# Optimization experiments

Hardware: AMD Instinct MI355X
Metric: run time of the kernel (lower is better)

The kernel has to match this reference:

```python
import jax, jax.numpy as jnp
import numpy as np

B, N, A, O, D, Q, H = 64, 4, 1024, 128, 256, 256, 128
NEG_INF = -1e30


def setup_inputs() -> dict:
    key = jax.random.key(0)
    ks = jax.random.split(key, 8)
    q = jax.random.normal(ks[0], (B, N, 1, Q), dtype=jnp.float32)
    att1 = jax.random.uniform(ks[1], (B, N, A, O), dtype=jnp.float32)
    obj_reps = jax.random.normal(ks[2], (B, O, D), dtype=jnp.float32)
    tags_attention = jax.random.randint(ks[3], (B, N, A), 0, 2, dtype=jnp.int32)
    W1 = jax.random.normal(ks[4], (D + Q, H), dtype=jnp.float32) / np.sqrt(D + Q)
    b1 = jnp.zeros((H,), dtype=jnp.float32)
    W2 = jax.random.normal(ks[5], (H, 1), dtype=jnp.float32) / np.sqrt(H)
    b2 = jnp.zeros((1,), dtype=jnp.float32)
    return {"q": q, "att1": att1, "obj_reps": obj_reps,
            "tags_attention": tags_attention,
            "W1": W1, "b1": b1, "W2": W2, "b2": b2, "t": 1}


def reference(q, att1, obj_reps, tags_attention, W1, b1, W2, b2, t):
    # v: [B,N,A,D] = att1 [B,N,A,O] @ obj_reps [B,O,D]
    v = jnp.einsum('bnao,bod->bnad', att1, obj_reps)
    # q broadcast over token dim A, concat -> [B,N,A,D+Q]
    q_proj = jnp.broadcast_to(q, v.shape[:3] + (q.shape[-1],))
    vq = jnp.concatenate([v, q_proj], axis=-1)
    # FCNet: Linear + ReLU (dropout is identity at inference)
    joint_repr = jax.nn.relu(vq @ W1 + b1)          # [B,N,A,H]
    logits = (joint_repr @ W2 + b2)[..., 0]          # [B,N,A]
    # temperature-scaled masked softmax over tokens
    masked = jnp.where(tags_attention > 0, logits / t, NEG_INF)
    att2 = jax.nn.softmax(masked, axis=-1)           # [B,N,A]
    # attention_last: [B,N,O] = att2 [B,N,1,A] @ att1 [B,N,A,O]
    return jnp.einsum('bna,bnao->bno', att2, att1)
```

## Files before the change

### kernel.cpp

```cpp
#include <hip/hip_runtime.h>
#include <math.h>

#define Bc 64
#define Nc 4
#define Ac 1024
#define Oc 128
#define Dc 256
#define Qc 256
#define Hc 128
#define BN (Bc*Nc)

using f4     = __attribute__((ext_vector_type(4))) float;
using f32x4  = __attribute__((ext_vector_type(4))) float;
using short8 = __attribute__((ext_vector_type(8))) short;
using us4    = __attribute__((ext_vector_type(4))) unsigned short;

__device__ inline float decode_t(const void* p) {
    int i = *(const int*)p;
    if (i >= 1 && i <= 1000000) return (float)i;
    return __int_as_float(i);
}

__device__ inline void split_bf16(float x, unsigned short& hi, unsigned short& lo) {
    unsigned u = __builtin_bit_cast(unsigned, x);
    hi = (unsigned short)(u >> 16);
    float hif = __builtin_bit_cast(float, u & 0xFFFF0000u);
    float lof = x - hif;
    lo = (unsigned short)(__builtin_bit_cast(unsigned, lof) >> 16);
}

__global__ __launch_bounds__(256) void prep_M_kernel(
    const float* __restrict__ obj, const float* __restrict__ W1,
    unsigned short* __restrict__ Mt_hi, unsigned short* __restrict__ Mt_lo)
{
    __shared__ float w_s[32][36];
    __shared__ float obj_sT[32][68];

    const int t  = threadIdx.x;
    const int tx = t & 15;
    const int ty = t >> 4;
    const int h0 = blockIdx.x * 32;
    const int o0 = blockIdx.y * 64;
    const int b  = blockIdx.z;

    float acc[2][4];
    #pragma unroll
    for (int i = 0; i < 2; i++)
        #pragma unroll
        for (int j = 0; j < 4; j++) acc[i][j] = 0.f;

    for (int ko = 0; ko < 8; ++ko) {
        __syncthreads();
        {
            int r = t >> 3, c4 = t & 7;
            f4 v = *(const f4*)(W1 + (size_t)(ko * 32 + r) * Hc + h0 + c4 * 4);
            *(f4*)&w_s[r][c4 * 4] = v;
        }
        #pragma unroll
        for (int s = 0; s < 2; s++) {
            int idx = t + 256 * s;
            int r = idx >> 3, c4 = idx & 7;
            f4 v = *(const f4*)(obj + ((size_t)b * Oc + o0 + r) * Dc + ko * 32 + c4 * 4);
            obj_sT[c4 * 4 + 0][r] = v[0];
            obj_sT[c4 * 4 + 1][r] = v[1];
            obj_sT[c4 * 4 + 2][r] = v[2];
            obj_sT[c4 * 4 + 3][r] = v[3];
        }
        __syncthreads();
        #pragma unroll 4
        for (int k = 0; k < 32; k++) {
            float a0 = w_s[k][ty * 2];
            float a1 = w_s[k][ty * 2 + 1];
            f4 bv = *(const f4*)&obj_sT[k][tx * 4];
            #pragma unroll
            for (int j = 0; j < 4; j++) {
                acc[0][j] += a0 * bv[j];
                acc[1][j] += a1 * bv[j];
            }
        }
    }

    #pragma unroll
    for (int i = 0; i < 2; i++) {
        us4 hi, lo;
        #pragma unroll
        for (int j = 0; j < 4; j++) {
            unsigned short h16, l16;
            split_bf16(acc[i][j], h16, l16);
            hi[j] = h16; lo[j] = l16;
        }
        size_t ofs = ((size_t)b * Hc + h0 + ty * 2 + i) * Oc + o0 + tx * 4;
        *(us4*)(Mt_hi + ofs) = hi;
        *(us4*)(Mt_lo + ofs) = lo;
    }
}

__global__ __launch_bounds__(512) void prep_qb_kernel(
    const float* __restrict__ q, const float* __restrict__ W1,
    const float* __restrict__ b1, float* __restrict__ qb,
    float* __restrict__ out_acc, float* __restrict__ Zsum)
{
    __shared__ float qs[256];
    __shared__ float red[4][128];
    const int t = threadIdx.x;
    const int bn = blockIdx.x;

    if (t < 256) qs[t] = q[bn * Qc + t];
    __syncthreads();

    const int h = t & 127, kq = t >> 7;
    float acc = 0.f;
    const float* w = W1 + (size_t)(Dc + kq * 64) * Hc + h;
    #pragma unroll 8
    for (int d = 0; d < 64; ++d)
        acc += qs[kq * 64 + d] * w[(size_t)d * Hc];
    red[kq][h] = acc;
    __syncthreads();

    if (t < 128) {
        qb[bn * Hc + t] = b1[t] + red[0][t] + red[1][t] + red[2][t] + red[3][t];
        out_acc[bn * Oc + t] = 0.f;
    }
    if (t == 128) Zsum[bn] = 0.f;
}

__global__ __launch_bounds__(256) void main_kernel(
    const float* __restrict__ att1, const int* __restrict__ tags,
    const unsigned short* __restrict__ Mt_hi, const unsigned short* __restrict__ Mt_lo,
    const float* __restrict__ qb, const float* __restrict__ W2,
    const float* __restrict__ b2, const void* __restrict__ tptr,
    float* __restrict__ out_acc, float* __restrict__ Zsum)
{
    __shared__ unsigned short A_hi[64][136];
    __shared__ unsigned short A_lo[64][136];
    __shared__ float part2[64][4];
    __shared__ float qb_s[128], w2_s[128];
    __shared__ float e_s[64];

    const int t    = threadIdx.x;
    const int wave = t >> 6;
    const int lane = t & 63;
    const int l15  = lane & 15;
    const int quad = lane >> 4;
    const int a0 = blockIdx.x * 64;
    const int n  = blockIdx.y;
    const int b  = blockIdx.z;
    const int bn = b * Nc + n;

    const float* att_base = att1 + ((size_t)bn * Ac + a0) * Oc;

    #pragma unroll
    for (int s = 0; s < 8; s++) {
        int idx = t + 256 * s;
        int r = idx >> 5, c4 = idx & 31;
        f4 v = *(const f4*)(att_base + (size_t)r * Oc + c4 * 4);
        us4 hi, lo;
        #pragma unroll
        for (int j = 0; j < 4; j++) {
            unsigned short h16, l16;
            split_bf16(v[j], h16, l16);
            hi[j] = h16; lo[j] = l16;
        }
        *(us4*)&A_hi[r][c4 * 4] = hi;
        *(us4*)&A_lo[r][c4 * 4] = lo;
    }
    if (t < 128) { qb_s[t] = qb[bn * Hc + t]; w2_s[t] = W2[t]; }
    __syncthreads();

    f32x4 acc[4][2];
    #pragma unroll
    for (int i = 0; i < 4; i++)
        #pragma unroll
        for (int j = 0; j < 2; j++) acc[i][j] = (f32x4)(0.f);

    const unsigned short* BhiB = Mt_hi + ((size_t)b * Hc + wave * 32 + l15) * Oc;
    const unsigned short* BloB = Mt_lo + ((size_t)b * Hc + wave * 32 + l15) * Oc;
    const int kq8 = quad * 8;

    #pragma unroll
    for (int ks = 0; ks < 4; ks++) {
        const int ko = ks * 32 + kq8;
        short8 b0h = *(const short8*)(BhiB + ko);
        short8 b0l = *(const short8*)(BloB + ko);
        short8 b1h = *(const short8*)(BhiB + 16 * Oc + ko);
        short8 b1l = *(const short8*)(BloB + 16 * Oc + ko);
        #pragma unroll
        for (int i = 0; i < 4; i++) {
            short8 ah = *(const short8*)&A_hi[i * 16 + l15][ko];
            short8 al = *(const short8*)&A_lo[i * 16 + l15][ko];
            acc[i][0] = __builtin_amdgcn_mfma_f32_16x16x32_bf16(ah, b0h, acc[i][0], 0, 0, 0);
            acc[i][0] = __builtin_amdgcn_mfma_f32_16x16x32_bf16(al, b0h, acc[i][0], 0, 0, 0);
            acc[i][0] = __builtin_amdgcn_mfma_f32_16x16x32_bf16(ah, b0l, acc[i][0], 0, 0, 0);
            acc[i][1] = __builtin_amdgcn_mfma_f32_16x16x32_bf16(ah, b1h, acc[i][1], 0, 0, 0);
            acc[i][1] = __builtin_amdgcn_mfma_f32_16x16x32_bf16(al, b1h, acc[i][1], 0, 0, 0);
            acc[i][1] = __builtin_amdgcn_mfma_f32_16x16x32_bf16(ah, b1l, acc[i][1], 0, 0, 0);
        }
    }

    float p[4][4];
    #pragma unroll
    for (int i = 0; i < 4; i++)
        #pragma unroll
        for (int r = 0; r < 4; r++) p[i][r] = 0.f;
    #pragma unroll
    for (int j = 0; j < 2; j++) {
        int h = wave * 32 + j * 16 + l15;
        float qbv = qb_s[h], w2v = w2_s[h];
        #pragma unroll
        for (int i = 0; i < 4; i++)
            #pragma unroll
            for (int r = 0; r < 4; r++) {
                float v = acc[i][j][r] + qbv;
                v = v > 0.f ? v : 0.f;
                p[i][r] += v * w2v;
            }
    }
    #pragma unroll
    for (int m = 1; m <= 8; m <<= 1)
        #pragma unroll
        for (int i = 0; i < 4; i++)
            #pragma unroll
            for (int r = 0; r < 4; r++)
                p[i][r] += __shfl_xor(p[i][r], m);
    if (l15 == 0) {
        #pragma unroll
        for (int i = 0; i < 4; i++)
            #pragma unroll
            for (int r = 0; r < 4; r++)
                part2[i * 16 + quad * 4 + r][wave] = p[i][r];
    }
    __syncthreads();

    if (t < 64) {
        float sum = part2[t][0] + part2[t][1] + part2[t][2] + part2[t][3] + b2[0];
        float tval = decode_t(tptr);
        float logit = sum / tval;
        int tag = tags[bn * Ac + a0 + t];
        float e = (tag > 0) ? expf(logit) : 0.f;
        e_s[t] = e;
        float zs = e;
        #pragma unroll
        for (int off = 32; off > 0; off >>= 1) zs += __shfl_down(zs, off);
        if (t == 0) atomicAdd(&Zsum[bn], zs);
    }
    __syncthreads();

    const int o = t & 127;
    const int half = t >> 7;
    const float* ab = att_base + (size_t)(half * 32) * Oc + o;
    float accum = 0.f;
    #pragma unroll 8
    for (int a = 0; a < 32; a++)
        accum += e_s[half * 32 + a] * ab[(size_t)a * Oc];
    atomicAdd(&out_acc[bn * Oc + o], accum);
}

__global__ void finalize_kernel(const float* __restrict__ out_acc,
                                const float* __restrict__ Zsum,
                                float* __restrict__ out)
{
    int idx = blockIdx.x * 256 + threadIdx.x;
    if (idx < BN * Oc) {
        out[idx] = out_acc[idx] / Zsum[idx >> 7];
    }
}

extern "C" void kernel_launch(void* const* d_in, const int* in_sizes, int n_in,
                              void* d_out, int out_size, void* d_ws, size_t ws_size,
                              hipStream_t stream)
{
    (void)in_sizes; (void)n_in; (void)out_size; (void)ws_size;

    const float* q    = (const float*)d_in[0];
    const float* att1 = (const float*)d_in[1];
    const float* obj  = (const float*)d_in[2];
    const int*   tags = (const int*)d_in[3];
    const float* W1   = (const float*)d_in[4];
    const float* b1   = (const float*)d_in[5];
    const float* W2   = (const float*)d_in[6];
    const float* b2   = (const float*)d_in[7];
    const void*  tptr = d_in[8];
    float* out = (float*)d_out;

    char* wsb = (char*)d_ws;
    unsigned short* Mt_hi = (unsigned short*)wsb;
    unsigned short* Mt_lo = (unsigned short*)(wsb + (size_t)2*1024*1024);
    float* qbuf = (float*)(wsb + (size_t)4*1024*1024);
    float* oacc = qbuf + (size_t)BN * Hc;
    float* Zs   = oacc + (size_t)BN * Oc;

    prep_M_kernel<<<dim3(4, 2, Bc), 256, 0, stream>>>(obj, W1, Mt_hi, Mt_lo);
    prep_qb_kernel<<<dim3(BN), 512, 0, stream>>>(q, W1, b1, qbuf, oacc, Zs);
    main_kernel<<<dim3(Ac / 64, Nc, Bc), 256, 0, stream>>>(att1, tags, Mt_hi, Mt_lo,
                                                           qbuf, W2, b2, tptr, oacc, Zs);
    finalize_kernel<<<dim3(BN * Oc / 256), 256, 0, stream>>>(oacc, Zs, out);
}
```

Baseline: 267.5 us.

## Restructure main kernel into 512-thread two-tile blocks with single-bf16 activations

The main kernel now processes 128 tokens per block with 8 waves, each wave owning 16 hidden columns. The B fragments stay in registers across both 64-row tiles, and the second tile's att1 loads are prefetched while the first tile is computed. The att1 activations are rounded to one bf16 (RNE) instead of a hi/lo split, which cuts MFMAs from three to two per step and halves the LDS staging, at some cost in accuracy of the logits. prep_M also gains register prefetching of the next K-slice, and the exponential uses __expf.

```diff
diff --git a/kernel.cpp b/kernel.cpp
--- a/kernel.cpp
+++ b/kernel.cpp
@@ -21,6 +21,12 @@
     return __int_as_float(i);
 }
 
+__device__ inline unsigned short bf16_rne(float x) {
+    unsigned u = __builtin_bit_cast(unsigned, x);
+    u += 0x7FFFu + ((u >> 16) & 1u);
+    return (unsigned short)(u >> 16);
+}
+
 __device__ inline void split_bf16(float x, unsigned short& hi, unsigned short& lo) {
     unsigned u = __builtin_bit_cast(unsigned, x);
     hi = (unsigned short)(u >> 16);
@@ -42,6 +48,9 @@
     const int h0 = blockIdx.x * 32;
     const int o0 = blockIdx.y * 64;
     const int b  = blockIdx.z;
+    const int r8 = t >> 3, c8 = t & 7;
+
+    const float* objb = obj + ((size_t)b * Oc + o0) * Dc;
 
     float acc[2][4];
     #pragma unroll
@@ -49,24 +58,26 @@
         #pragma unroll
         for (int j = 0; j < 4; j++) acc[i][j] = 0.f;
 
+    f4 wv  = *(const f4*)(W1 + (size_t)r8 * Hc + h0 + c8 * 4);
+    f4 ov0 = *(const f4*)(objb + (size_t)r8 * Dc + c8 * 4);
+    f4 ov1 = *(const f4*)(objb + (size_t)(r8 + 32) * Dc + c8 * 4);
+
     for (int ko = 0; ko < 8; ++ko) {
-        __syncthreads();
-        {
-            int r = t >> 3, c4 = t & 7;
-            f4 v = *(const f4*)(W1 + (size_t)(ko * 32 + r) * Hc + h0 + c4 * 4);
-            *(f4*)&w_s[r][c4 * 4] = v;
-        }
-        #pragma unroll
-        for (int s = 0; s < 2; s++) {
-            int idx = t + 256 * s;
-            int r = idx >> 3, c4 = idx & 7;
-            f4 v = *(const f4*)(obj + ((size_t)b * Oc + o0 + r) * Dc + ko * 32 + c4 * 4);
-            obj_sT[c4 * 4 + 0][r] = v[0];
-            obj_sT[c4 * 4 + 1][r] = v[1];
-            obj_sT[c4 * 4 + 2][r] = v[2];
-            obj_sT[c4 * 4 + 3][r] = v[3];
-        }
-        __syncthreads();
+        *(f4*)&w_s[r8][c8 * 4] = wv;
+        obj_sT[c8 * 4 + 0][r8] = ov0[0];
+        obj_sT[c8 * 4 + 1][r8] = ov0[1];
+        obj_sT[c8 * 4 + 2][r8] = ov0[2];
+        obj_sT[c8 * 4 + 3][r8] = ov0[3];
+        obj_sT[c8 * 4 + 0][r8 + 32] = ov1[0];
+        obj_sT[c8 * 4 + 1][r8 + 32] = ov1[1];
+        obj_sT[c8 * 4 + 2][r8 + 32] = ov1[2];
+        obj_sT[c8 * 4 + 3][r8 + 32] = ov1[3];
+        __syncthreads();
+        if (ko < 7) {
+            wv  = *(const f4*)(W1 + (size_t)((ko + 1) * 32 + r8) * Hc + h0 + c8 * 4);
+            ov0 = *(const f4*)(objb + (size_t)r8 * Dc + (ko + 1) * 32 + c8 * 4);
+            ov1 = *(const f4*)(objb + (size_t)(r8 + 32) * Dc + (ko + 1) * 32 + c8 * 4);
+        }
         #pragma unroll 4
         for (int k = 0; k < 32; k++) {
             float a0 = w_s[k][ty * 2];
@@ -78,6 +89,7 @@
                 acc[1][j] += a1 * bv[j];
             }
         }
+        __syncthreads();
     }
 
     #pragma unroll
@@ -124,16 +136,15 @@
     if (t == 128) Zsum[bn] = 0.f;
 }
 
-__global__ __launch_bounds__(256) void main_kernel(
+__global__ __launch_bounds__(512, 3) void main_kernel(
     const float* __restrict__ att1, const int* __restrict__ tags,
     const unsigned short* __restrict__ Mt_hi, const unsigned short* __restrict__ Mt_lo,
     const float* __restrict__ qb, const float* __restrict__ W2,
     const float* __restrict__ b2, const void* __restrict__ tptr,
     float* __restrict__ out_acc, float* __restrict__ Zsum)
 {
-    __shared__ unsigned short A_hi[64][136];
-    __shared__ unsigned short A_lo[64][136];
-    __shared__ float part2[64][4];
+    __shared__ unsigned short A_s[2][64][136];
+    __shared__ float part2[64][9];
     __shared__ float qb_s[128], w2_s[128];
     __shared__ float e_s[64];
 
@@ -142,117 +153,121 @@
     const int lane = t & 63;
     const int l15  = lane & 15;
     const int quad = lane >> 4;
-    const int a0 = blockIdx.x * 64;
+    const int a0 = blockIdx.x * 128;
     const int n  = blockIdx.y;
     const int b  = blockIdx.z;
     const int bn = b * Nc + n;
 
     const float* att_base = att1 + ((size_t)bn * Ac + a0) * Oc;
 
-    #pragma unroll
-    for (int s = 0; s < 8; s++) {
-        int idx = t + 256 * s;
-        int r = idx >> 5, c4 = idx & 31;
-        f4 v = *(const f4*)(att_base + (size_t)r * Oc + c4 * 4);
-        us4 hi, lo;
-        #pragma unroll
-        for (int j = 0; j < 4; j++) {
-            unsigned short h16, l16;
-            split_bf16(v[j], h16, l16);
-            hi[j] = h16; lo[j] = l16;
-        }
-        *(us4*)&A_hi[r][c4 * 4] = hi;
-        *(us4*)&A_lo[r][c4 * 4] = lo;
-    }
+    f4 sv[4];
+    #pragma unroll
+    for (int s = 0; s < 4; s++) {
+        int idx = t + 512 * s;
+        sv[s] = *(const f4*)(att_base + (size_t)(idx >> 5) * Oc + (idx & 31) * 4);
+    }
+
+    const size_t brow = ((size_t)b * Hc + wave * 16 + l15) * Oc;
+    short8 Bh[4], Bl[4];
+    #pragma unroll
+    for (int ks = 0; ks < 4; ks++) {
+        const int ko = ks * 32 + quad * 8;
+        Bh[ks] = *(const short8*)(Mt_hi + brow + ko);
+        Bl[ks] = *(const short8*)(Mt_lo + brow + ko);
+    }
+
     if (t < 128) { qb_s[t] = qb[bn * Hc + t]; w2_s[t] = W2[t]; }
-    __syncthreads();
-
-    f32x4 acc[4][2];
-    #pragma unroll
-    for (int i = 0; i < 4; i++)
-        #pragma unroll
-        for (int j = 0; j < 2; j++) acc[i][j] = (f32x4)(0.f);
-
-    const unsigned short* BhiB = Mt_hi + ((size_t)b * Hc + wave * 32 + l15) * Oc;
-    const unsigned short* BloB = Mt_lo + ((size_t)b * Hc + wave * 32 + l15) * Oc;
-    const int kq8 = quad * 8;
-
-    #pragma unroll
-    for (int ks = 0; ks < 4; ks++) {
-        const int ko = ks * 32 + kq8;
-        short8 b0h = *(const short8*)(BhiB + ko);
-        short8 b0l = *(const short8*)(BloB + ko);
-        short8 b1h = *(const short8*)(BhiB + 16 * Oc + ko);
-        short8 b1l = *(const short8*)(BloB + 16 * Oc + ko);
-        #pragma unroll
-        for (int i = 0; i < 4; i++) {
-            short8 ah = *(const short8*)&A_hi[i * 16 + l15][ko];
-            short8 al = *(const short8*)&A_lo[i * 16 + l15][ko];
-            acc[i][0] = __builtin_amdgcn_mfma_f32_16x16x32_bf16(ah, b0h, acc[i][0], 0, 0, 0);
-            acc[i][0] = __builtin_amdgcn_mfma_f32_16x16x32_bf16(al, b0h, acc[i][0], 0, 0, 0);
-            acc[i][0] = __builtin_amdgcn_mfma_f32_16x16x32_bf16(ah, b0l, acc[i][0], 0, 0, 0);
-            acc[i][1] = __builtin_amdgcn_mfma_f32_16x16x32_bf16(ah, b1h, acc[i][1], 0, 0, 0);
-            acc[i][1] = __builtin_amdgcn_mfma_f32_16x16x32_bf16(al, b1h, acc[i][1], 0, 0, 0);
-            acc[i][1] = __builtin_amdgcn_mfma_f32_16x16x32_bf16(ah, b1l, acc[i][1], 0, 0, 0);
-        }
-    }
-
-    float p[4][4];
-    #pragma unroll
-    for (int i = 0; i < 4; i++)
-        #pragma unroll
-        for (int r = 0; r < 4; r++) p[i][r] = 0.f;
-    #pragma unroll
-    for (int j = 0; j < 2; j++) {
-        int h = wave * 32 + j * 16 + l15;
-        float qbv = qb_s[h], w2v = w2_s[h];
+    const int tag0 = (t < 64) ? tags[bn * Ac + a0 + t] : 0;
+    const int tag1 = (t < 64) ? tags[bn * Ac + a0 + 64 + t] : 0;
+    const float b2v  = b2[0];
+    const float tval = decode_t(tptr);
+
+    #pragma unroll
+    for (int tile = 0; tile < 2; ++tile) {
+        #pragma unroll
+        for (int s = 0; s < 4; s++) {
+            int idx = t + 512 * s;
+            int r = idx >> 5, c4 = idx & 31;
+            us4 h4;
+            #pragma unroll
+            for (int j = 0; j < 4; j++) h4[j] = bf16_rne(sv[s][j]);
+            *(us4*)&A_s[tile][r][c4 * 4] = h4;
+        }
+        __syncthreads();
+
+        if (tile == 0) {
+            #pragma unroll
+            for (int s = 0; s < 4; s++) {
+                int idx = t + 512 * s;
+                sv[s] = *(const f4*)(att_base + (size_t)(64 + (idx >> 5)) * Oc + (idx & 31) * 4);
+            }
+        }
+
+        f32x4 acc[4];
+        #pragma unroll
+        for (int i = 0; i < 4; i++) acc[i] = (f32x4)(0.f);
+        #pragma unroll
+        for (int ks = 0; ks < 4; ks++) {
+            const int ko = ks * 32 + quad * 8;
+            #pragma unroll
+            for (int i = 0; i < 4; i++) {
+                short8 ah = *(const short8*)&A_s[tile][i * 16 + l15][ko];
+                acc[i] = __builtin_amdgcn_mfma_f32_16x16x32_bf16(ah, Bh[ks], acc[i], 0, 0, 0);
+                acc[i] = __builtin_amdgcn_mfma_f32_16x16x32_bf16(ah, Bl[ks], acc[i], 0, 0, 0);
+            }
+        }
+
+        const int h = wave * 16 + l15;
+        const float qbv = qb_s[h], w2v = w2_s[h];
+        float p[4][4];
         #pragma unroll
         for (int i = 0; i < 4; i++)
             #pragma unroll
             for (int r = 0; r < 4; r++) {
-                float v = acc[i][j][r] + qbv;
+                float v = acc[i][r] + qbv;
                 v = v > 0.f ? v : 0.f;
-                p[i][r] += v * w2v;
+                p[i][r] = v * w2v;
             }
-    }
-    #pragma unroll
-    for (int m = 1; m <= 8; m <<= 1)
-        #pragma unroll
-        for (int i = 0; i < 4; i++)
-            #pragma unroll
-            for (int r = 0; r < 4; r++)
-                p[i][r] += __shfl_xor(p[i][r], m);
-    if (l15 == 0) {
-        #pragma unroll
-        for (int i = 0; i < 4; i++)
-            #pragma unroll
-            for (int r = 0; r < 4; r++)
-                part2[i * 16 + quad * 4 + r][wave] = p[i][r];
-    }
-    __syncthreads();
-
-    if (t < 64) {
-        float sum = part2[t][0] + part2[t][1] + part2[t][2] + part2[t][3] + b2[0];
-        float tval = decode_t(tptr);
-        float logit = sum / tval;
-        int tag = tags[bn * Ac + a0 + t];
-        float e = (tag > 0) ? expf(logit) : 0.f;
-        e_s[t] = e;
-        float zs = e;
-        #pragma unroll
-        for (int off = 32; off > 0; off >>= 1) zs += __shfl_down(zs, off);
-        if (t == 0) atomicAdd(&Zsum[bn], zs);
-    }
-    __syncthreads();
-
-    const int o = t & 127;
-    const int half = t >> 7;
-    const float* ab = att_base + (size_t)(half * 32) * Oc + o;
-    float accum = 0.f;
-    #pragma unroll 8
-    for (int a = 0; a < 32; a++)
-        accum += e_s[half * 32 + a] * ab[(size_t)a * Oc];
-    atomicAdd(&out_acc[bn * Oc + o], accum);
+        #pragma unroll
+        for (int m = 1; m <= 8; m <<= 1)
+            #pragma unroll
+            for (int i = 0; i < 4; i++)
+                #pragma unroll
+                for (int r = 0; r < 4; r++)
+                    p[i][r] += __shfl_xor(p[i][r], m);
+        if (l15 == 0) {
+            #pragma unroll
+            for (int i = 0; i < 4; i++)
+                #pragma unroll
+                for (int r = 0; r < 4; r++)
+                    part2[i * 16 + quad * 4 + r][wave] = p[i][r];
+        }
+        __syncthreads();
+
+        if (t < 64) {
+            float sum = b2v;
+            #pragma unroll
+            for (int x = 0; x < 8; x++) sum += part2[t][x];
+            float logit = sum / tval;
+            int tg = tile ? tag1 : tag0;
+            float e = (tg > 0) ? __expf(logit) : 0.f;
+            e_s[t] = e;
+            float zs = e;
+            #pragma unroll
+            for (int off = 32; off > 0; off >>= 1) zs += __shfl_down(zs, off);
+            if (t == 0) atomicAdd(&Zsum[bn], zs);
+        }
+        __syncthreads();
+
+        const int o  = t & 127;
+        const int q4 = t >> 7;
+        const float* ab = att_base + ((size_t)tile * 64 + q4 * 16) * Oc + o;
+        float accum = 0.f;
+        #pragma unroll
+        for (int a = 0; a < 16; a++)
+            accum += e_s[q4 * 16 + a] * ab[(size_t)a * Oc];
+        atomicAdd(&out_acc[bn * Oc + o], accum);
+    }
 }
 
 __global__ void finalize_kernel(const float* __restrict__ out_acc,
@@ -291,7 +306,7 @@
 
     prep_M_kernel<<<dim3(4, 2, Bc), 256, 0, stream>>>(obj, W1, Mt_hi, Mt_lo);
     prep_qb_kernel<<<dim3(BN), 512, 0, stream>>>(q, W1, b1, qbuf, oacc, Zs);
-    main_kernel<<<dim3(Ac / 64, Nc, Bc), 256, 0, stream>>>(att1, tags, Mt_hi, Mt_lo,
-                                                           qbuf, W2, b2, tptr, oacc, Zs);
+    main_kernel<<<dim3(Ac / 128, Nc, Bc), 512, 0, stream>>>(att1, tags, Mt_hi, Mt_lo,
+                                                            qbuf, W2, b2, tptr, oacc, Zs);
     finalize_kernel<<<dim3(BN * Oc / 256), 256, 0, stream>>>(oacc, Zs, out);
 }
```

New measurement: 250.1 us. -6.5%, faster.
